# Optimization experiments

Hardware: AMD Instinct MI355X
Metric: run time of the kernel (lower is better)

The kernel has to match this reference:

```python
import jax, jax.numpy as jnp
import numpy as np

B, T, N, F, H, H2, OUT = 32, 24, 256, 16, 128, 64, 24


def setup_inputs() -> dict:
    key = jax.random.key(0)
    ks = jax.random.split(key, 12)
    p = lambda k, shp: (jax.random.normal(k, shp, jnp.float32) * 0.05)
    x = jax.random.normal(ks[0], (B, T, N, F), jnp.float32)
    # positive adjacency weights, row-scaled by N to keep aggregation well-conditioned
    adj = jax.random.uniform(ks[1], (B, T, N, N), jnp.float32) / jnp.float32(N)
    return {
        "x": x,
        "adj": adj,
        "target_station_idx": 5,
        "gcn_W": p(ks[2], (F + H, 4 * H)),
        "gcn_b": jnp.zeros((4 * H,), jnp.float32),
        "gru_Wih": p(ks[3], (3 * H, F)),
        "gru_Whh": p(ks[4], (3 * H, H)),
        "gru_bih": jnp.zeros((3 * H,), jnp.float32),
        "gru_bhh": jnp.zeros((3 * H,), jnp.float32),
        "fc2_W": p(ks[5], (H, 2 * H)),
        "fc2_b": jnp.zeros((H,), jnp.float32),
        "fc3_W": p(ks[6], (H2, H)),
        "fc3_b": jnp.zeros((H2,), jnp.float32),
        "fc4_W": p(ks[7], (OUT, H2)),
        "fc4_b": jnp.zeros((OUT,), jnp.float32),
        "fc5_W": p(ks[8], (H, H)),
        "fc5_b": jnp.zeros((H,), jnp.float32),
    }


def reference(x, adj, target_station_idx, gcn_W, gcn_b, gru_Wih, gru_Whh,
              gru_bih, gru_bhh, fc2_W, fc2_b, fc3_W, fc3_b, fc4_W, fc4_b,
              fc5_W, fc5_b):
    A = adj[:, -1]  # [B, N, N] -- only last-timestep adjacency is used

    # --- spatial branch: graph-conv LSTM cell scanned over time ---
    def gcn_step(carry, x_t):
        h, c = carry                                  # [B, N, H] each
        xh = jnp.concatenate([x_t, h], axis=-1)       # [B, N, F+H]
        agg = jnp.einsum('bij,bjf->bif', A, xh)       # neighborhood aggregation
        gates = agg @ gcn_W + gcn_b                   # [B, N, 4H]
        i, f, g, o = jnp.split(gates, 4, axis=-1)
        c = jax.nn.sigmoid(f) * c + jax.nn.sigmoid(i) * jnp.tanh(g)
        h = jax.nn.sigmoid(o) * jnp.tanh(c)
        return (h, c), None

    h0 = jnp.zeros((B, N, H), x.dtype)
    (h_sp, _), _ = jax.lax.scan(gcn_step, (h0, jnp.zeros_like(h0)),
                                jnp.moveaxis(x, 1, 0))  # scan over T
    x_spatial = jax.nn.relu(h_sp) @ fc5_W.T + fc5_b     # [B, N, H]
    x_spatial = x_spatial[:, target_station_idx]        # [B, H]

    # --- temporal branch: torch-style GRU over target station ---
    xt = x[:, :, target_station_idx, :]                 # [B, T, F]

    def gru_step(h, x_t):
        gi = x_t @ gru_Wih.T + gru_bih
        gh = h @ gru_Whh.T + gru_bhh
        ir, iz, inn = jnp.split(gi, 3, axis=-1)
        hr, hz, hn = jnp.split(gh, 3, axis=-1)
        r = jax.nn.sigmoid(ir + hr)
        z = jax.nn.sigmoid(iz + hz)
        n = jnp.tanh(inn + r * hn)
        return (1.0 - z) * n + z * h, None

    h_tmp, _ = jax.lax.scan(gru_step, jnp.zeros((B, H), x.dtype),
                            jnp.moveaxis(xt, 1, 0))     # [B, H] (last step)

    # --- fusion + MLP head ---
    hc = jnp.concatenate([h_tmp, x_spatial], axis=-1)   # [B, 2H]
    hc = jax.nn.relu(hc @ fc2_W.T + fc2_b)
    out_ = jax.nn.relu(hc @ fc3_W.T + fc3_b)
    return out_ @ fc4_W.T + fc4_b                       # [B, output_len]
```

## Files before the change

kernel.cpp:

```cpp
#include <hip/hip_runtime.h>
#include <math.h>

#define BB 32
#define TT 24
#define NN 256
#define FF 16
#define HH 128
#define G4 512

typedef _Float16 half8 __attribute__((ext_vector_type(8)));
typedef float f32x4 __attribute__((ext_vector_type(4)));

__device__ __forceinline__ float sigf(float x) { return 1.f / (1.f + __expf(-x)); }
__device__ __forceinline__ float tanhfast(float x) { return 1.f - 2.f / (__expf(2.f * x) + 1.f); }

__device__ __forceinline__ void split8(const float* v, half8& hi, half8& lo) {
#pragma unroll
  for (int i = 0; i < 8; ++i) {
    const _Float16 h = (_Float16)v[i];
    hi[i] = h;
    lo[i] = (_Float16)(v[i] - (float)h);
  }
}

__global__ __launch_bounds__(64) void k0_wswz(const float* __restrict__ gcnW,
                                              _Float16* __restrict__ WfH,
                                              _Float16* __restrict__ WfL) {
  const int bid = blockIdx.x;
  const int kc = bid >> 5, ct = bid & 31;
  const int l = threadIdx.x, quad = l >> 4, lo16 = l & 15;
  float v[8];
#pragma unroll
  for (int j = 0; j < 8; ++j) {
    const int k = quad * 8 + j;
    float val = 0.f;
    if (kc < 4) val = gcnW[(size_t)(16 + kc * 32 + k) * G4 + ct * 16 + lo16];
    else if (k < 16) val = gcnW[(size_t)k * G4 + ct * 16 + lo16];
    v[j] = val;
  }
  half8 hi, lo;
  split8(v, hi, lo);
  const size_t off = (size_t)bid * 512 + l * 8;
  *(half8*)&WfH[off] = hi;
  *(half8*)&WfL[off] = lo;
}

__global__ __launch_bounds__(64) void k0_aswz(const float* __restrict__ adj,
                                              _Float16* __restrict__ AfH,
                                              _Float16* __restrict__ AfL) {
  const int nt16 = blockIdx.x >> 3, kc = blockIdx.x & 7;
  const int b = blockIdx.y;
  const int l = threadIdx.x, quad = l >> 4, lo16 = l & 15;
  const float* src =
      adj + (((size_t)(b * TT + TT - 1)) * NN + nt16 * 16 + lo16) * NN + kc * 32 + quad * 8;
  const float4 v0 = *(const float4*)src;
  const float4 v1 = *(const float4*)(src + 4);
  float v[8] = {v0.x, v0.y, v0.z, v0.w, v1.x, v1.y, v1.z, v1.w};
  half8 hi, lo;
  split8(v, hi, lo);
  const size_t off = (((size_t)b * 16 + nt16) * 8 + kc) * 512 + l * 8;
  *(half8*)&AfH[off] = hi;
  *(half8*)&AfL[off] = lo;
}

__global__ __launch_bounds__(256) void k1_ax(const float* __restrict__ adj,
                                             const float* __restrict__ x,
                                             float* __restrict__ Ax) {
  const int bt = blockIdx.x;
  const int b = bt / TT;
  const float* Abase = adj + ((size_t)(b * TT + (TT - 1)) * NN) * NN;
  const float* xbase = x + (size_t)bt * NN * FF;

  __shared__ float x_s[NN * FF];
  __shared__ float A_s[64 * 65];

  for (int i4 = threadIdx.x; i4 < (NN * FF) / 4; i4 += 256) {
    ((float4*)x_s)[i4] = ((const float4*)xbase)[i4];
  }
  const int rg = threadIdx.x >> 2;
  const int fg = threadIdx.x & 3;

  for (int rt = 0; rt < 4; ++rt) {
    float4 acc = make_float4(0.f, 0.f, 0.f, 0.f);
    for (int jc = 0; jc < 4; ++jc) {
      __syncthreads();
      for (int i = threadIdx.x; i < 64 * 64; i += 256) {
        const int r = i >> 6, j = i & 63;
        A_s[r * 65 + j] = Abase[(size_t)(rt * 64 + r) * NN + jc * 64 + j];
      }
      __syncthreads();
#pragma unroll 8
      for (int j = 0; j < 64; ++j) {
        const float a = A_s[rg * 65 + j];
        const float4 xv = *(const float4*)&x_s[(jc * 64 + j) * FF + fg * 4];
        acc.x += a * xv.x;
        acc.y += a * xv.y;
        acc.z += a * xv.z;
        acc.w += a * xv.w;
      }
    }
    *(float4*)&Ax[((size_t)bt * NN + rt * 64 + rg) * FF + fg * 4] = acc;
  }
}

__global__ __launch_bounds__(256, 2) void k2_step(
    const _Float16* __restrict__ AfH, const _Float16* __restrict__ AfL,
    const _Float16* __restrict__ WfH, const _Float16* __restrict__ WfL,
    const float* __restrict__ Ax, const float* __restrict__ gcnb,
    const _Float16* __restrict__ hInH, const _Float16* __restrict__ hInL,
    _Float16* __restrict__ hOutH, _Float16* __restrict__ hOutL,
    float* __restrict__ cbuf, float* __restrict__ h32, int t) {
  const int nt = blockIdx.x, b = blockIdx.y;
  const int n0 = nt * 32;
  const int tid = threadIdx.x;
  const int w = tid >> 6, l = tid & 63, quad = l >> 4, lo16 = l & 15;

  __shared__ float region[16512];

  {
    const int r = tid >> 3, f = (tid & 7) * 2;
    const float2 v = *(const float2*)&Ax[(((size_t)(b * TT + t)) * NN + n0 + r) * FF + f];
    *(float2*)&region[r * 164 + 128 + f] = v;
    *(float2*)&region[r * 164 + 144 + f] = make_float2(0.f, 0.f);
  }

  f32x4 accA[2][2];
#pragma unroll
  for (int rt = 0; rt < 2; ++rt)
#pragma unroll
    for (int cc = 0; cc < 2; ++cc) accA[rt][cc] = (f32x4){0.f, 0.f, 0.f, 0.f};

  for (int kc = 0; kc < 8; ++kc) {
    half8 aH[2], aL[2], bH[2], bL[2];
#pragma unroll
    for (int rt = 0; rt < 2; ++rt) {
      const size_t off = (((size_t)b * 16 + 2 * nt + rt) * 8 + kc) * 512 + l * 8;
      aH[rt] = *(const half8*)&AfH[off];
      aL[rt] = *(const half8*)&AfL[off];
    }
#pragma unroll
    for (int cc = 0; cc < 2; ++cc) {
      const size_t off = (((size_t)b * 8 + kc) * 8 + (w * 2 + cc)) * 512 + l * 8;
      bH[cc] = *(const half8*)&hInH[off];
      bL[cc] = *(const half8*)&hInL[off];
    }
#pragma unroll
    for (int rt = 0; rt < 2; ++rt)
#pragma unroll
      for (int cc = 0; cc < 2; ++cc) {
        accA[rt][cc] = __builtin_amdgcn_mfma_f32_16x16x32_f16(aL[rt], bH[cc], accA[rt][cc], 0, 0, 0);
        accA[rt][cc] = __builtin_amdgcn_mfma_f32_16x16x32_f16(aH[rt], bL[cc], accA[rt][cc], 0, 0, 0);
        accA[rt][cc] = __builtin_amdgcn_mfma_f32_16x16x32_f16(aH[rt], bH[cc], accA[rt][cc], 0, 0, 0);
      }
  }
#pragma unroll
  for (int rt = 0; rt < 2; ++rt)
#pragma unroll
    for (int cc = 0; cc < 2; ++cc)
#pragma unroll
      for (int r = 0; r < 4; ++r)
        region[(rt * 16 + quad * 4 + r) * 164 + (w * 2 + cc) * 16 + lo16] = accA[rt][cc][r];
  __syncthreads();

  f32x4 acc[2][8];
#pragma unroll
  for (int rt = 0; rt < 2; ++rt)
#pragma unroll
    for (int cc = 0; cc < 8; ++cc) acc[rt][cc] = (f32x4){0.f, 0.f, 0.f, 0.f};

  for (int kc = 0; kc < 5; ++kc) {
    half8 pH[2], pL[2];
#pragma unroll
    for (int rt = 0; rt < 2; ++rt) {
      const float* src = &region[(rt * 16 + lo16) * 164 + kc * 32 + quad * 8];
      const float4 v0 = *(const float4*)src;
      const float4 v1 = *(const float4*)(src + 4);
      float av[8] = {v0.x, v0.y, v0.z, v0.w, v1.x, v1.y, v1.z, v1.w};
      split8(av, pH[rt], pL[rt]);
    }
#pragma unroll
    for (int cc = 0; cc < 8; ++cc) {
      const size_t woff = ((size_t)(kc * 32 + w * 8 + cc)) * 512 + l * 8;
      const half8 wH = *(const half8*)&WfH[woff];
      const half8 wL = *(const half8*)&WfL[woff];
#pragma unroll
      for (int rt = 0; rt < 2; ++rt) {
        acc[rt][cc] = __builtin_amdgcn_mfma_f32_16x16x32_f16(pL[rt], wH, acc[rt][cc], 0, 0, 0);
        acc[rt][cc] = __builtin_amdgcn_mfma_f32_16x16x32_f16(pH[rt], wL, acc[rt][cc], 0, 0, 0);
        acc[rt][cc] = __builtin_amdgcn_mfma_f32_16x16x32_f16(pH[rt], wH, acc[rt][cc], 0, 0, 0);
      }
    }
  }
  __syncthreads();
#pragma unroll
  for (int rt = 0; rt < 2; ++rt)
#pragma unroll
    for (int cc = 0; cc < 8; ++cc)
#pragma unroll
      for (int r = 0; r < 4; ++r)
        region[(rt * 16 + quad * 4 + r) * 516 + (w * 8 + cc) * 16 + lo16] = acc[rt][cc][r];
  __syncthreads();

  const int node = tid >> 3, hg = tid & 7;
  float hv[16];
  union F4 { float4 v; float a[4]; };
#pragma unroll
  for (int q = 0; q < 4; ++q) {
    const int col = hg * 16 + q * 4;
    F4 gi, gf, gg, go, c4, bi, bf, bg, bo, cn, hn;
    gi.v = *(const float4*)&region[node * 516 + col];
    gf.v = *(const float4*)&region[node * 516 + 128 + col];
    gg.v = *(const float4*)&region[node * 516 + 256 + col];
    go.v = *(const float4*)&region[node * 516 + 384 + col];
    bi.v = *(const float4*)&gcnb[col];
    bf.v = *(const float4*)&gcnb[128 + col];
    bg.v = *(const float4*)&gcnb[256 + col];
    bo.v = *(const float4*)&gcnb[384 + col];
    const size_t coff = ((size_t)b * NN + n0 + node) * HH + col;
    c4.v = *(const float4*)&cbuf[coff];
#pragma unroll
    for (int c = 0; c < 3 + 1; ++c) {
      const float iv = sigf(gi.a[c] + bi.a[c]);
      const float fv = sigf(gf.a[c] + bf.a[c]);
      const float gv = tanhfast(gg.a[c] + bg.a[c]);
      const float ov = sigf(go.a[c] + bo.a[c]);
      const float cnew = fv * c4.a[c] + iv * gv;
      cn.a[c] = cnew;
      hn.a[c] = ov * tanhfast(cnew);
      hv[q * 4 + c] = hn.a[c];
    }
    *(float4*)&cbuf[coff] = cn.v;
    if (nt == 0) *(float4*)&h32[((size_t)b * 32 + node) * HH + col] = hn.v;
  }
  __syncthreads();
#pragma unroll
  for (int j = 0; j < 8; ++j)
    *(float2*)&region[node * 130 + hg * 16 + 2 * j] = make_float2(hv[2 * j], hv[2 * j + 1]);
  __syncthreads();
#pragma unroll
  for (int cc = 0; cc < 2; ++cc) {
    const int ct = w * 2 + cc;
    float v[8];
#pragma unroll
    for (int j = 0; j < 8; ++j) v[j] = region[(quad * 8 + j) * 130 + ct * 16 + lo16];
    half8 hh, hl;
    split8(v, hh, hl);
    const size_t off = (((size_t)b * 8 + nt) * 8 + ct) * 512 + l * 8;
    *(half8*)&hOutH[off] = hh;
    *(half8*)&hOutL[off] = hl;
  }
}

__global__ __launch_bounds__(384) void k_tail(
    const float* __restrict__ x, const float* __restrict__ h32,
    const int* __restrict__ tsi_p, const float* __restrict__ gruWih,
    const float* __restrict__ gruWhh, const float* __restrict__ gru_bih,
    const float* __restrict__ gru_bhh, const float* __restrict__ fc2W,
    const float* __restrict__ fc2b, const float* __restrict__ fc3W,
    const float* __restrict__ fc3b, const float* __restrict__ fc4W,
    const float* __restrict__ fc4b, const float* __restrict__ fc5W,
    const float* __restrict__ fc5b, float* __restrict__ out) {
  const int b = blockIdx.x;
  const int m = threadIdx.x;
  const int tsi = tsi_p[0];

  __shared__ float h_s[HH];
  __shared__ float xts[TT * FF];
  __shared__ float sum_s[384];
  __shared__ float gh_s[384];
  __shared__ float hc_s[2 * HH];
  __shared__ float xr_s[HH];
  __shared__ float f2_s[HH];
  __shared__ float f3_s[64];

  float4 whh[32];
#pragma unroll
  for (int q = 0; q < 32; ++q) whh[q] = *(const float4*)&gruWhh[(size_t)m * HH + q * 4];
  float4 wih[4];
#pragma unroll
  for (int q = 0; q < 4; ++q) wih[q] = *(const float4*)&gruWih[(size_t)m * FF + q * 4];
  const float bih_r = gru_bih[m];
  const float bhh_r = gru_bhh[m];

  {
    const int t = m >> 4, f = m & 15;
    xts[m] = x[(((size_t)b * TT + t) * NN + tsi) * FF + f];
  }
  if (m < HH) h_s[m] = 0.f;
  __syncthreads();

  for (int t = 0; t < TT; ++t) {
    float gi = bih_r;
#pragma unroll
    for (int q = 0; q < 4; ++q) {
      const float4 xv = *(const float4*)&xts[t * FF + q * 4];
      gi += wih[q].x * xv.x + wih[q].y * xv.y + wih[q].z * xv.z + wih[q].w * xv.w;
    }
    float gh = bhh_r;
#pragma unroll
    for (int q = 0; q < 32; ++q) {
      const float4 hv = *(const float4*)&h_s[q * 4];
      gh += whh[q].x * hv.x + whh[q].y * hv.y + whh[q].z * hv.z + whh[q].w * hv.w;
    }
    sum_s[m] = gi + gh;
    gh_s[m] = gh;
    __syncthreads();
    float hnew = 0.f;
    if (m < HH) {
      const float r = sigf(sum_s[m]);
      const float z = sigf(sum_s[HH + m]);
      const float ghn = gh_s[2 * HH + m];
      const float nn = tanhfast(sum_s[2 * HH + m] - ghn + r * ghn);
      hnew = (1.f - z) * nn + z * h_s[m];
    }
    __syncthreads();
    if (m < HH) h_s[m] = hnew;
    __syncthreads();
  }

  if (m < HH) {
    hc_s[m] = h_s[m];
    xr_s[m] = fmaxf(h32[((size_t)b * 32 + tsi) * HH + m], 0.f);
  }
  __syncthreads();
  if (m < HH) {
    float v = fc5b[m];
    const float* wr = fc5W + (size_t)m * HH;
#pragma unroll 8
    for (int k = 0; k < HH; k += 4) {
      const float4 wv = *(const float4*)(wr + k);
      v += xr_s[k] * wv.x + xr_s[k + 1] * wv.y + xr_s[k + 2] * wv.z + xr_s[k + 3] * wv.w;
    }
    hc_s[HH + m] = v;
  }
  __syncthreads();
  if (m < HH) {
    float v = fc2b[m];
    const float* wr = fc2W + (size_t)m * 2 * HH;
#pragma unroll 8
    for (int k = 0; k < 2 * HH; k += 4) {
      const float4 wv = *(const float4*)(wr + k);
      v += hc_s[k] * wv.x + hc_s[k + 1] * wv.y + hc_s[k + 2] * wv.z + hc_s[k + 3] * wv.w;
    }
    f2_s[m] = fmaxf(v, 0.f);
  }
  __syncthreads();
  if (m < 64) {
    float v = fc3b[m];
    const float* wr = fc3W + (size_t)m * HH;
#pragma unroll 8
    for (int k = 0; k < HH; k += 4) {
      const float4 wv = *(const float4*)(wr + k);
      v += f2_s[k] * wv.x + f2_s[k + 1] * wv.y + f2_s[k + 2] * wv.z + f2_s[k + 3] * wv.w;
    }
    f3_s[m] = fmaxf(v, 0.f);
  }
  __syncthreads();
  if (m < 24) {
    float v = fc4b[m];
    const float* wr = fc4W + (size_t)m * 64;
#pragma unroll
    for (int k = 0; k < 64; k += 4) {
      const float4 wv = *(const float4*)(wr + k);
      v += f3_s[k] * wv.x + f3_s[k + 1] * wv.y + f3_s[k + 2] * wv.z + f3_s[k + 3] * wv.w;
    }
    out[b * 24 + m] = v;
  }
}

extern "C" void kernel_launch(void* const* d_in, const int* in_sizes, int n_in,
                              void* d_out, int out_size, void* d_ws, size_t ws_size,
                              hipStream_t stream) {
  const float* x = (const float*)d_in[0];
  const float* adj = (const float*)d_in[1];
  const int* tsi = (const int*)d_in[2];
  const float* gcnW = (const float*)d_in[3];
  const float* gcnb = (const float*)d_in[4];
  const float* gruWih = (const float*)d_in[5];
  const float* gruWhh = (const float*)d_in[6];
  const float* gru_bih = (const float*)d_in[7];
  const float* gru_bhh = (const float*)d_in[8];
  const float* fc2W = (const float*)d_in[9];
  const float* fc2b = (const float*)d_in[10];
  const float* fc3W = (const float*)d_in[11];
  const float* fc3b = (const float*)d_in[12];
  const float* fc4W = (const float*)d_in[13];
  const float* fc4b = (const float*)d_in[14];
  const float* fc5W = (const float*)d_in[15];
  const float* fc5b = (const float*)d_in[16];
  float* out = (float*)d_out;

  float* Ax = (float*)d_ws;
  float* cbuf = Ax + 3145728;
  _Float16* hfH0 = (_Float16*)(cbuf + 1048576);
  _Float16* hfL0 = hfH0 + 1048576;
  _Float16* hfH1 = hfL0 + 1048576;
  _Float16* hfL1 = hfH1 + 1048576;
  float* h32 = (float*)(hfL1 + 1048576);
  _Float16* AfH = (_Float16*)(h32 + 131072);
  _Float16* AfL = AfH + 2097152;
  _Float16* WfH = AfL + 2097152;
  _Float16* WfL = WfH + 81920;

  hipMemsetAsync(cbuf, 0, 1048576 * 4 + 2 * 1048576 * 2, stream);

  k0_wswz<<<dim3(160), 64, 0, stream>>>(gcnW, WfH, WfL);
  k0_aswz<<<dim3(128, BB), 64, 0, stream>>>(adj, AfH, AfL);
  k1_ax<<<dim3(BB * TT), 256, 0, stream>>>(adj, x, Ax);

  for (int t = 0; t < TT; ++t) {
    const _Float16* hiH = (t & 1) ? hfH1 : hfH0;
    const _Float16* hiL = (t & 1) ? hfL1 : hfL0;
    _Float16* hoH = (t & 1) ? hfH0 : hfH1;
    _Float16* hoL = (t & 1) ? hfL0 : hfL1;
    k2_step<<<dim3(8, BB), 256, 0, stream>>>(AfH, AfL, WfH, WfL, Ax, gcnb, hiH, hiL, hoH, hoL,
                                             cbuf, h32, t);
  }
  k_tail<<<dim3(BB), 384, 0, stream>>>(x, h32, tsi, gruWih, gruWhh, gru_bih, gru_bhh, fc2W,
                                       fc2b, fc3W, fc3b, fc4W, fc4b, fc5W, fc5b, out);
}
```

Before: 929.4 us.

## Fuse GCN-LSTM time loop into one persistent kernel with per-batch spin barriers

Replaces the adjacency swizzle, the A·x precompute and the 24 per-step launches with a single persistent kernel of 512 blocks (16 per batch, 16 nodes each). Each block keeps its adjacency rows as split-fp16 fragments in registers and the cell state c in registers, and computes A·x in shared memory at the start. Between time steps the 16 blocks of a batch synchronise through an atomic counter spin barrier. This removes launch overhead and the global round-trips for c, Ax and the swizzled adjacency. It relies on all 512 blocks being co-resident to avoid deadlock, and the smaller per-block tile reduces MFMA reuse of the weights.

```diff
diff --git a/kernel.cpp b/kernel.cpp
--- a/kernel.cpp
+++ b/kernel.cpp
@@ -25,7 +25,12 @@
 
 __global__ __launch_bounds__(64) void k0_wswz(const float* __restrict__ gcnW,
                                               _Float16* __restrict__ WfH,
-                                              _Float16* __restrict__ WfL) {
+                                              _Float16* __restrict__ WfL,
+                                              unsigned* __restrict__ cnt) {
+  if (blockIdx.x == 0) {
+#pragma unroll
+    for (int i = 0; i < 8; ++i) cnt[threadIdx.x + 64 * i] = 0u;
+  }
   const int bid = blockIdx.x;
   const int kc = bid >> 5, ct = bid & 31;
   const int l = threadIdx.x, quad = l >> 4, lo16 = l & 15;
@@ -45,209 +50,190 @@
   *(half8*)&WfL[off] = lo;
 }
 
-__global__ __launch_bounds__(64) void k0_aswz(const float* __restrict__ adj,
-                                              _Float16* __restrict__ AfH,
-                                              _Float16* __restrict__ AfL) {
-  const int nt16 = blockIdx.x >> 3, kc = blockIdx.x & 7;
-  const int b = blockIdx.y;
-  const int l = threadIdx.x, quad = l >> 4, lo16 = l & 15;
-  const float* src =
-      adj + (((size_t)(b * TT + TT - 1)) * NN + nt16 * 16 + lo16) * NN + kc * 32 + quad * 8;
-  const float4 v0 = *(const float4*)src;
-  const float4 v1 = *(const float4*)(src + 4);
-  float v[8] = {v0.x, v0.y, v0.z, v0.w, v1.x, v1.y, v1.z, v1.w};
-  half8 hi, lo;
-  split8(v, hi, lo);
-  const size_t off = (((size_t)b * 16 + nt16) * 8 + kc) * 512 + l * 8;
-  *(half8*)&AfH[off] = hi;
-  *(half8*)&AfL[off] = lo;
-}
-
-__global__ __launch_bounds__(256) void k1_ax(const float* __restrict__ adj,
-                                             const float* __restrict__ x,
-                                             float* __restrict__ Ax) {
-  const int bt = blockIdx.x;
-  const int b = bt / TT;
-  const float* Abase = adj + ((size_t)(b * TT + (TT - 1)) * NN) * NN;
-  const float* xbase = x + (size_t)bt * NN * FF;
-
-  __shared__ float x_s[NN * FF];
-  __shared__ float A_s[64 * 65];
-
-  for (int i4 = threadIdx.x; i4 < (NN * FF) / 4; i4 += 256) {
-    ((float4*)x_s)[i4] = ((const float4*)xbase)[i4];
-  }
-  const int rg = threadIdx.x >> 2;
-  const int fg = threadIdx.x & 3;
-
-  for (int rt = 0; rt < 4; ++rt) {
-    float4 acc = make_float4(0.f, 0.f, 0.f, 0.f);
-    for (int jc = 0; jc < 4; ++jc) {
-      __syncthreads();
-      for (int i = threadIdx.x; i < 64 * 64; i += 256) {
-        const int r = i >> 6, j = i & 63;
-        A_s[r * 65 + j] = Abase[(size_t)(rt * 64 + r) * NN + jc * 64 + j];
-      }
-      __syncthreads();
-#pragma unroll 8
-      for (int j = 0; j < 64; ++j) {
-        const float a = A_s[rg * 65 + j];
-        const float4 xv = *(const float4*)&x_s[(jc * 64 + j) * FF + fg * 4];
-        acc.x += a * xv.x;
-        acc.y += a * xv.y;
-        acc.z += a * xv.z;
-        acc.w += a * xv.w;
-      }
-    }
-    *(float4*)&Ax[((size_t)bt * NN + rt * 64 + rg) * FF + fg * 4] = acc;
-  }
-}
-
-__global__ __launch_bounds__(256, 2) void k2_step(
-    const _Float16* __restrict__ AfH, const _Float16* __restrict__ AfL,
+#define AH_OFF 0
+#define GS_OFF 2112
+#define HS_OFF 10368
+#define AX_OFF 12448
+#define SMEM_F 18592
+
+__global__ __launch_bounds__(256, 2) void k_fused(
+    const float* __restrict__ adj, const float* __restrict__ x,
     const _Float16* __restrict__ WfH, const _Float16* __restrict__ WfL,
-    const float* __restrict__ Ax, const float* __restrict__ gcnb,
-    const _Float16* __restrict__ hInH, const _Float16* __restrict__ hInL,
-    _Float16* __restrict__ hOutH, _Float16* __restrict__ hOutL,
-    float* __restrict__ cbuf, float* __restrict__ h32, int t) {
-  const int nt = blockIdx.x, b = blockIdx.y;
-  const int n0 = nt * 32;
+    const float* __restrict__ gcnb, _Float16* __restrict__ hfH0,
+    _Float16* __restrict__ hfL0, _Float16* __restrict__ hfH1,
+    _Float16* __restrict__ hfL1, float* __restrict__ h32,
+    unsigned* __restrict__ cnt) {
+  const int bid = blockIdx.x;
+  const int b = bid >> 4, nt = bid & 15;
+  const int n0 = nt * 16;
   const int tid = threadIdx.x;
   const int w = tid >> 6, l = tid & 63, quad = l >> 4, lo16 = l & 15;
 
-  __shared__ float region[16512];
-
+  __shared__ float smem[SMEM_F];
+  float* Ah_s = smem + AH_OFF;
+  float* g_s = smem + GS_OFF;
+  float* hst = smem + HS_OFF;
+  float* Ax_s = smem + AX_OFF;
+
+  half8 afH[8], afL[8];
   {
-    const int r = tid >> 3, f = (tid & 7) * 2;
-    const float2 v = *(const float2*)&Ax[(((size_t)(b * TT + t)) * NN + n0 + r) * FF + f];
-    *(float2*)&region[r * 164 + 128 + f] = v;
-    *(float2*)&region[r * 164 + 144 + f] = make_float2(0.f, 0.f);
-  }
-
-  f32x4 accA[2][2];
-#pragma unroll
-  for (int rt = 0; rt < 2; ++rt)
-#pragma unroll
-    for (int cc = 0; cc < 2; ++cc) accA[rt][cc] = (f32x4){0.f, 0.f, 0.f, 0.f};
-
-  for (int kc = 0; kc < 8; ++kc) {
-    half8 aH[2], aL[2], bH[2], bL[2];
-#pragma unroll
-    for (int rt = 0; rt < 2; ++rt) {
-      const size_t off = (((size_t)b * 16 + 2 * nt + rt) * 8 + kc) * 512 + l * 8;
-      aH[rt] = *(const half8*)&AfH[off];
-      aL[rt] = *(const half8*)&AfL[off];
-    }
-#pragma unroll
-    for (int cc = 0; cc < 2; ++cc) {
-      const size_t off = (((size_t)b * 8 + kc) * 8 + (w * 2 + cc)) * 512 + l * 8;
-      bH[cc] = *(const half8*)&hInH[off];
-      bL[cc] = *(const half8*)&hInL[off];
-    }
-#pragma unroll
-    for (int rt = 0; rt < 2; ++rt)
-#pragma unroll
-      for (int cc = 0; cc < 2; ++cc) {
-        accA[rt][cc] = __builtin_amdgcn_mfma_f32_16x16x32_f16(aL[rt], bH[cc], accA[rt][cc], 0, 0, 0);
-        accA[rt][cc] = __builtin_amdgcn_mfma_f32_16x16x32_f16(aH[rt], bL[cc], accA[rt][cc], 0, 0, 0);
-        accA[rt][cc] = __builtin_amdgcn_mfma_f32_16x16x32_f16(aH[rt], bH[cc], accA[rt][cc], 0, 0, 0);
-      }
-  }
-#pragma unroll
-  for (int rt = 0; rt < 2; ++rt)
+    const float* Abase = adj + ((size_t)(b * TT + TT - 1) * NN + n0 + lo16) * NN;
+#pragma unroll
+    for (int kc = 0; kc < 8; ++kc) {
+      const float4 p0 = *(const float4*)(Abase + kc * 32 + quad * 8);
+      const float4 p1 = *(const float4*)(Abase + kc * 32 + quad * 8 + 4);
+      float v[8] = {p0.x, p0.y, p0.z, p0.w, p1.x, p1.y, p1.z, p1.w};
+      split8(v, afH[kc], afL[kc]);
+    }
+  }
+  const int node = tid >> 4, colg = (tid & 15) * 8;
+  float bia[4][8];
+#pragma unroll
+  for (int g = 0; g < 4; ++g) {
+    *(float4*)&bia[g][0] = *(const float4*)&gcnb[g * HH + colg];
+    *(float4*)&bia[g][4] = *(const float4*)&gcnb[g * HH + colg + 4];
+  }
+  float c[8];
+#pragma unroll
+  for (int j = 0; j < 8; ++j) c[j] = 0.f;
+
+  for (int t = w; t < TT; t += 4) {
+    f32x4 acc = (f32x4){0.f, 0.f, 0.f, 0.f};
+    const float* xb = x + ((size_t)(b * TT + t)) * NN * FF;
+    for (int kc = 0; kc < 8; ++kc) {
+      float v[8];
+#pragma unroll
+      for (int j = 0; j < 8; ++j) v[j] = xb[(kc * 32 + quad * 8 + j) * FF + lo16];
+      half8 xH, xL;
+      split8(v, xH, xL);
+      acc = __builtin_amdgcn_mfma_f32_16x16x32_f16(afL[kc], xH, acc, 0, 0, 0);
+      acc = __builtin_amdgcn_mfma_f32_16x16x32_f16(afH[kc], xL, acc, 0, 0, 0);
+      acc = __builtin_amdgcn_mfma_f32_16x16x32_f16(afH[kc], xH, acc, 0, 0, 0);
+    }
+#pragma unroll
+    for (int r = 0; r < 4; ++r) Ax_s[t * 256 + (quad * 4 + r) * 16 + lo16] = acc[r];
+  }
+  __syncthreads();
+
+  const size_t hfbase = (size_t)b * 64 * 512;
+
+  for (int t = 0; t < TT; ++t) {
+    f32x4 accA[2];
+    accA[0] = (f32x4){0.f, 0.f, 0.f, 0.f};
+    accA[1] = (f32x4){0.f, 0.f, 0.f, 0.f};
+    if (t > 0) {
+      const _Float16* hH = (t & 1) ? hfH1 : hfH0;
+      const _Float16* hL = (t & 1) ? hfL1 : hfL0;
+      for (int kc = 0; kc < 8; ++kc) {
+        const size_t o0 = hfbase + ((size_t)kc * 8 + 2 * w) * 512 + l * 8;
+        const half8 bH0 = *(const half8*)&hH[o0];
+        const half8 bL0 = *(const half8*)&hL[o0];
+        const half8 bH1 = *(const half8*)&hH[o0 + 512];
+        const half8 bL1 = *(const half8*)&hL[o0 + 512];
+        accA[0] = __builtin_amdgcn_mfma_f32_16x16x32_f16(afL[kc], bH0, accA[0], 0, 0, 0);
+        accA[0] = __builtin_amdgcn_mfma_f32_16x16x32_f16(afH[kc], bL0, accA[0], 0, 0, 0);
+        accA[0] = __builtin_amdgcn_mfma_f32_16x16x32_f16(afH[kc], bH0, accA[0], 0, 0, 0);
+        accA[1] = __builtin_amdgcn_mfma_f32_16x16x32_f16(afL[kc], bH1, accA[1], 0, 0, 0);
+        accA[1] = __builtin_amdgcn_mfma_f32_16x16x32_f16(afH[kc], bL1, accA[1], 0, 0, 0);
+        accA[1] = __builtin_amdgcn_mfma_f32_16x16x32_f16(afH[kc], bH1, accA[1], 0, 0, 0);
+      }
+    }
 #pragma unroll
     for (int cc = 0; cc < 2; ++cc)
 #pragma unroll
       for (int r = 0; r < 4; ++r)
-        region[(rt * 16 + quad * 4 + r) * 164 + (w * 2 + cc) * 16 + lo16] = accA[rt][cc][r];
-  __syncthreads();
-
-  f32x4 acc[2][8];
-#pragma unroll
-  for (int rt = 0; rt < 2; ++rt)
-#pragma unroll
-    for (int cc = 0; cc < 8; ++cc) acc[rt][cc] = (f32x4){0.f, 0.f, 0.f, 0.f};
-
-  for (int kc = 0; kc < 5; ++kc) {
-    half8 pH[2], pL[2];
-#pragma unroll
-    for (int rt = 0; rt < 2; ++rt) {
-      const float* src = &region[(rt * 16 + lo16) * 164 + kc * 32 + quad * 8];
-      const float4 v0 = *(const float4*)src;
-      const float4 v1 = *(const float4*)(src + 4);
-      float av[8] = {v0.x, v0.y, v0.z, v0.w, v1.x, v1.y, v1.z, v1.w};
-      split8(av, pH[rt], pL[rt]);
-    }
-#pragma unroll
-    for (int cc = 0; cc < 8; ++cc) {
-      const size_t woff = ((size_t)(kc * 32 + w * 8 + cc)) * 512 + l * 8;
-      const half8 wH = *(const half8*)&WfH[woff];
-      const half8 wL = *(const half8*)&WfL[woff];
-#pragma unroll
-      for (int rt = 0; rt < 2; ++rt) {
-        acc[rt][cc] = __builtin_amdgcn_mfma_f32_16x16x32_f16(pL[rt], wH, acc[rt][cc], 0, 0, 0);
-        acc[rt][cc] = __builtin_amdgcn_mfma_f32_16x16x32_f16(pH[rt], wL, acc[rt][cc], 0, 0, 0);
-        acc[rt][cc] = __builtin_amdgcn_mfma_f32_16x16x32_f16(pH[rt], wH, acc[rt][cc], 0, 0, 0);
-      }
-    }
-  }
-  __syncthreads();
-#pragma unroll
-  for (int rt = 0; rt < 2; ++rt)
+        Ah_s[(quad * 4 + r) * 132 + (2 * w + cc) * 16 + lo16] = accA[cc][r];
+    __syncthreads();
+
+    f32x4 acc[8];
+#pragma unroll
+    for (int cc = 0; cc < 8; ++cc) acc[cc] = (f32x4){0.f, 0.f, 0.f, 0.f};
+    for (int kc = 0; kc < 5; ++kc) {
+      half8 aH, aL;
+      if (kc < 4) {
+        const float* src = &Ah_s[lo16 * 132 + kc * 32 + quad * 8];
+        const float4 p0 = *(const float4*)src;
+        const float4 p1 = *(const float4*)(src + 4);
+        float v[8] = {p0.x, p0.y, p0.z, p0.w, p1.x, p1.y, p1.z, p1.w};
+        split8(v, aH, aL);
+      } else {
+        float v[8];
+        if (quad < 2) {
+#pragma unroll
+          for (int j = 0; j < 8; ++j) v[j] = Ax_s[t * 256 + lo16 * 16 + quad * 8 + j];
+        } else {
+#pragma unroll
+          for (int j = 0; j < 8; ++j) v[j] = 0.f;
+        }
+        split8(v, aH, aL);
+      }
+#pragma unroll
+      for (int cc = 0; cc < 8; ++cc) {
+        const size_t wo = ((size_t)(kc * 32 + w * 8 + cc)) * 512 + l * 8;
+        const half8 wH = *(const half8*)&WfH[wo];
+        const half8 wL = *(const half8*)&WfL[wo];
+        acc[cc] = __builtin_amdgcn_mfma_f32_16x16x32_f16(aL, wH, acc[cc], 0, 0, 0);
+        acc[cc] = __builtin_amdgcn_mfma_f32_16x16x32_f16(aH, wL, acc[cc], 0, 0, 0);
+        acc[cc] = __builtin_amdgcn_mfma_f32_16x16x32_f16(aH, wH, acc[cc], 0, 0, 0);
+      }
+    }
 #pragma unroll
     for (int cc = 0; cc < 8; ++cc)
 #pragma unroll
       for (int r = 0; r < 4; ++r)
-        region[(rt * 16 + quad * 4 + r) * 516 + (w * 8 + cc) * 16 + lo16] = acc[rt][cc][r];
-  __syncthreads();
-
-  const int node = tid >> 3, hg = tid & 7;
-  float hv[16];
-  union F4 { float4 v; float a[4]; };
-#pragma unroll
-  for (int q = 0; q < 4; ++q) {
-    const int col = hg * 16 + q * 4;
-    F4 gi, gf, gg, go, c4, bi, bf, bg, bo, cn, hn;
-    gi.v = *(const float4*)&region[node * 516 + col];
-    gf.v = *(const float4*)&region[node * 516 + 128 + col];
-    gg.v = *(const float4*)&region[node * 516 + 256 + col];
-    go.v = *(const float4*)&region[node * 516 + 384 + col];
-    bi.v = *(const float4*)&gcnb[col];
-    bf.v = *(const float4*)&gcnb[128 + col];
-    bg.v = *(const float4*)&gcnb[256 + col];
-    bo.v = *(const float4*)&gcnb[384 + col];
-    const size_t coff = ((size_t)b * NN + n0 + node) * HH + col;
-    c4.v = *(const float4*)&cbuf[coff];
-#pragma unroll
-    for (int c = 0; c < 3 + 1; ++c) {
-      const float iv = sigf(gi.a[c] + bi.a[c]);
-      const float fv = sigf(gf.a[c] + bf.a[c]);
-      const float gv = tanhfast(gg.a[c] + bg.a[c]);
-      const float ov = sigf(go.a[c] + bo.a[c]);
-      const float cnew = fv * c4.a[c] + iv * gv;
-      cn.a[c] = cnew;
-      hn.a[c] = ov * tanhfast(cnew);
-      hv[q * 4 + c] = hn.a[c];
-    }
-    *(float4*)&cbuf[coff] = cn.v;
-    if (nt == 0) *(float4*)&h32[((size_t)b * 32 + node) * HH + col] = hn.v;
-  }
-  __syncthreads();
-#pragma unroll
-  for (int j = 0; j < 8; ++j)
-    *(float2*)&region[node * 130 + hg * 16 + 2 * j] = make_float2(hv[2 * j], hv[2 * j + 1]);
-  __syncthreads();
-#pragma unroll
-  for (int cc = 0; cc < 2; ++cc) {
-    const int ct = w * 2 + cc;
-    float v[8];
-#pragma unroll
-    for (int j = 0; j < 8; ++j) v[j] = region[(quad * 8 + j) * 130 + ct * 16 + lo16];
-    half8 hh, hl;
-    split8(v, hh, hl);
-    const size_t off = (((size_t)b * 8 + nt) * 8 + ct) * 512 + l * 8;
-    *(half8*)&hOutH[off] = hh;
-    *(half8*)&hOutL[off] = hl;
+        g_s[(quad * 4 + r) * 516 + (w * 8 + cc) * 16 + lo16] = acc[cc][r];
+    __syncthreads();
+
+    float hv[8];
+#pragma unroll
+    for (int j = 0; j < 8; ++j) {
+      const float gi = g_s[node * 516 + 0 * HH + colg + j] + bia[0][j];
+      const float gf = g_s[node * 516 + 1 * HH + colg + j] + bia[1][j];
+      const float gg = g_s[node * 516 + 2 * HH + colg + j] + bia[2][j];
+      const float go = g_s[node * 516 + 3 * HH + colg + j] + bia[3][j];
+      const float cn = sigf(gf) * c[j] + sigf(gi) * tanhfast(gg);
+      c[j] = cn;
+      hv[j] = sigf(go) * tanhfast(cn);
+    }
+#pragma unroll
+    for (int j = 0; j < 8; ++j) hst[node * 130 + colg + j] = hv[j];
+    if (t == TT - 1) {
+      float* dst = &h32[((size_t)b * NN + n0 + node) * HH + colg];
+      *(float4*)dst = make_float4(hv[0], hv[1], hv[2], hv[3]);
+      *(float4*)(dst + 4) = make_float4(hv[4], hv[5], hv[6], hv[7]);
+    }
+    __syncthreads();
+
+    if (t < TT - 1) {
+      _Float16* oH = (t & 1) ? hfH0 : hfH1;
+      _Float16* oL = (t & 1) ? hfL0 : hfL1;
+      if ((l >> 5) == (nt & 1)) {
+        const int kq = quad - 2 * (nt & 1);
+#pragma unroll
+        for (int cc = 0; cc < 2; ++cc) {
+          const int ct = 2 * w + cc;
+          float v[8];
+#pragma unroll
+          for (int j = 0; j < 8; ++j) v[j] = hst[(kq * 8 + j) * 130 + ct * 16 + lo16];
+          half8 hh, hl;
+          split8(v, hh, hl);
+          const size_t o = hfbase + ((size_t)(nt >> 1) * 8 + ct) * 512 + l * 8;
+          *(half8*)&oH[o] = hh;
+          *(half8*)&oL[o] = hl;
+        }
+      }
+      __syncthreads();
+      if (tid == 0) {
+        __threadfence();
+        __hip_atomic_fetch_add(&cnt[b * 16], 1u, __ATOMIC_SEQ_CST, __HIP_MEMORY_SCOPE_AGENT);
+        const unsigned tgt = 16u * (unsigned)(t + 1);
+        while (__hip_atomic_load(&cnt[b * 16], __ATOMIC_SEQ_CST, __HIP_MEMORY_SCOPE_AGENT) < tgt) {
+          __builtin_amdgcn_s_sleep(2);
+        }
+        __threadfence();
+      }
+      __syncthreads();
+    }
   }
 }
 
@@ -320,7 +306,7 @@
 
   if (m < HH) {
     hc_s[m] = h_s[m];
-    xr_s[m] = fmaxf(h32[((size_t)b * 32 + tsi) * HH + m], 0.f);
+    xr_s[m] = fmaxf(h32[((size_t)b * NN + tsi) * HH + m], 0.f);
   }
   __syncthreads();
   if (m < HH) {
@@ -390,32 +376,18 @@
   const float* fc5b = (const float*)d_in[16];
   float* out = (float*)d_out;
 
-  float* Ax = (float*)d_ws;
-  float* cbuf = Ax + 3145728;
-  _Float16* hfH0 = (_Float16*)(cbuf + 1048576);
+  _Float16* WfH = (_Float16*)d_ws;
+  _Float16* WfL = WfH + 81920;
+  unsigned* cnt = (unsigned*)(WfL + 81920);
+  _Float16* hfH0 = (_Float16*)(cnt + 512);
   _Float16* hfL0 = hfH0 + 1048576;
   _Float16* hfH1 = hfL0 + 1048576;
   _Float16* hfL1 = hfH1 + 1048576;
   float* h32 = (float*)(hfL1 + 1048576);
-  _Float16* AfH = (_Float16*)(h32 + 131072);
-  _Float16* AfL = AfH + 2097152;
-  _Float16* WfH = AfL + 2097152;
-  _Float16* WfL = WfH + 81920;
-
-  hipMemsetAsync(cbuf, 0, 1048576 * 4 + 2 * 1048576 * 2, stream);
-
-  k0_wswz<<<dim3(160), 64, 0, stream>>>(gcnW, WfH, WfL);
-  k0_aswz<<<dim3(128, BB), 64, 0, stream>>>(adj, AfH, AfL);
-  k1_ax<<<dim3(BB * TT), 256, 0, stream>>>(adj, x, Ax);
-
-  for (int t = 0; t < TT; ++t) {
-    const _Float16* hiH = (t & 1) ? hfH1 : hfH0;
-    const _Float16* hiL = (t & 1) ? hfL1 : hfL0;
-    _Float16* hoH = (t & 1) ? hfH0 : hfH1;
-    _Float16* hoL = (t & 1) ? hfL0 : hfL1;
-    k2_step<<<dim3(8, BB), 256, 0, stream>>>(AfH, AfL, WfH, WfL, Ax, gcnb, hiH, hiL, hoH, hoL,
-                                             cbuf, h32, t);
-  }
+
+  k0_wswz<<<dim3(160), 64, 0, stream>>>(gcnW, WfH, WfL, cnt);
+  k_fused<<<dim3(512), 256, 0, stream>>>(adj, x, WfH, WfL, gcnb, hfH0, hfL0, hfH1, hfL1,
+                                         h32, cnt);
   k_tail<<<dim3(BB), 384, 0, stream>>>(x, h32, tsi, gruWih, gruWhh, gru_bih, gru_bhh, fc2W,
                                        fc2b, fc3W, fc3b, fc4W, fc4b, fc5W, fc5b, out);
 }
```

Result: slower. 2.463 ms (+165.0%).
